# Optimization experiments

Hardware: AMD Instinct MI355X
Metric: run time of the kernel (lower is better)

The kernel has to match this reference:

```python
import jax, jax.numpy as jnp
import numpy as np

B, N, D_MODEL, N_HEADS, WINDOW = 2, 2048, 1024, 16, 512
HEAD_DIM = D_MODEL // N_HEADS

def setup_inputs() -> dict:
    key = jax.random.key(0)
    k1, k2, k3 = jax.random.split(key, 3)
    x = jax.random.normal(k1, (B, N, D_MODEL), dtype=jnp.float32)
    W_qkv = jax.random.normal(k2, (D_MODEL, 3 * D_MODEL), dtype=jnp.float32) * 0.02
    W_proj = jax.random.normal(k3, (D_MODEL, D_MODEL), dtype=jnp.float32) * 0.02
    b_proj = jnp.zeros((D_MODEL,), dtype=jnp.float32)
    return {"x": x, "W_qkv": W_qkv, "W_proj": W_proj, "b_proj": b_proj}

def reference(x, W_qkv, W_proj, b_proj):
    Bx, Nx, C = x.shape
    H, Dh = N_HEADS, C // N_HEADS
    scale = Dh ** -0.5
    window = min(WINDOW, Nx)
    half = window // 2
    # qkv: [B,N,3C] -> [3,B,H,N,Dh]
    qkv = (x @ W_qkv).reshape(Bx, Nx, 3, H, Dh).transpose(2, 0, 3, 1, 4)
    q, k, v = qkv[0], qkv[1], qkv[2]
    # banded mask: allowed iff i-half <= j <= i+half
    i = jnp.arange(Nx)[:, None]
    j = jnp.arange(Nx)[None, :]
    allowed = jnp.abs(i - j) <= half  # [N,N] bool
    attn = jnp.einsum('bhqd,bhkd->bhqk', q, k) * scale
    attn = jnp.where(allowed[None, None], attn, -jnp.inf)
    attn = jax.nn.softmax(attn, axis=-1)
    out = jnp.einsum('bhqk,bhkd->bhqd', attn, v)
    out = out.transpose(0, 2, 1, 3).reshape(Bx, Nx, C)
    return out @ W_proj + b_proj
```

## Files before the change

### kernel.cpp

```cpp
#include <hip/hip_runtime.h>
#include <stdint.h>


typedef _Float16 f16x8 __attribute__((ext_vector_type(8)));
typedef _Float16 f16x4 __attribute__((ext_vector_type(4)));
typedef __fp16   fp16x2n __attribute__((ext_vector_type(2)));
typedef float    f32x2 __attribute__((ext_vector_type(2)));
typedef float    f32x4 __attribute__((ext_vector_type(4)));
typedef float    f32x16 __attribute__((ext_vector_type(16)));

#define MFMA16(a, b, c) __builtin_amdgcn_mfma_f32_16x16x32_f16((a), (b), (c), 0, 0, 0)
#define MFMA32(a, b, c) __builtin_amdgcn_mfma_f32_32x32x16_f16((a), (b), (c), 0, 0, 0)

__device__ __forceinline__ void gload16(const void* g, void* l) {
  __builtin_amdgcn_global_load_lds(
      (const __attribute__((address_space(1))) void*)g,
      (__attribute__((address_space(3))) void*)l, 16, 0, 0);
}

__device__ __forceinline__ unsigned pk2(float a, float b) {
  fp16x2n t = __builtin_amdgcn_cvt_pkrtz(a, b);
  return __builtin_bit_cast(unsigned, t);
}

__global__ __launch_bounds__(256) void prep(const float* __restrict__ x,
                                            const float* __restrict__ wqkv,
                                            const float* __restrict__ wproj,
                                            _Float16* __restrict__ Xb,
                                            _Float16* __restrict__ Wqt,
                                            _Float16* __restrict__ Wpt) {
  __shared__ float t[64][65];
  const int id = blockIdx.x, tid = threadIdx.x;
  if (id < 4096) {
    int i = (id * 256 + tid) * 4;
    float4 v = *(const float4*)(x + i);
    f16x4 h;
    h[0] = (_Float16)v.x; h[1] = (_Float16)v.y;
    h[2] = (_Float16)v.z; h[3] = (_Float16)v.w;
    *(f16x4*)(Xb + i) = h;
    return;
  }
  const float* in; _Float16* out; int N, bx, by;
  if (id < 4864) { int tt = id - 4096; in = wqkv; out = Wqt; N = 3072; bx = tt % 48; by = tt / 48; }
  else           { int tt = id - 4864; in = wproj; out = Wpt; N = 1024; bx = tt & 15; by = tt >> 4; }
  const int n0 = bx * 64, k0 = by * 64;
  {
    int j = tid & 63;
#pragma unroll
    for (int p = 0; p < 16; p++) {
      int i = p * 4 + (tid >> 6);
      t[i][j] = in[(size_t)(k0 + i) * N + n0 + j];
    }
  }
  __syncthreads();
  {
    int i = tid & 63;
#pragma unroll
    for (int p = 0; p < 16; p++) {
      int j = p * 4 + (tid >> 6);
      out[(size_t)(n0 + j) * 1024 + k0 + i] = (_Float16)t[i][j];
    }
  }
}

template <int BM, int BN, int EPI>
__global__ __launch_bounds__(256) void gemm16(const _Float16* __restrict__ A,
                                              const _Float16* __restrict__ Bt,
                                              const int K,
                                              _Float16* __restrict__ oh,
                                              _Float16* __restrict__ vt,
                                              float* __restrict__ of,
                                              const float* __restrict__ bias,
                                              const int Nout) {
  constexpr int RF = BM / 32, CF = BN / 32;
  constexpr int SLABS = (BM + BN) / 8;
  __shared__ __align__(16) char smem[(BM + BN) * 128];
  char* As = smem;
  char* Bs = smem + BM * 128;
  const int tid = threadIdx.x, wave = tid >> 6, lane = tid & 63;
  const int il = lane & 15, ih = lane >> 4;
  const int bm = blockIdx.y * BM, bn = blockIdx.x * BN;
  const int wm = wave >> 1, wn = wave & 1;
  const int rs = lane >> 3, cp = lane & 7;

  f32x4 acc[RF][CF] = {};

  for (int k0 = 0; k0 < K; k0 += 64) {
    __syncthreads();
#pragma unroll
    for (int s0 = 0; s0 < SLABS / 4; s0++) {
      int s = wave + s0 * 4;
      int row = s * 8 + rs;
      int c = cp ^ (row & 7);
      if (row < BM)
        gload16(A + (size_t)(bm + row) * K + k0 + c * 8, As + s * 1024);
      else
        gload16(Bt + (size_t)(bn + row - BM) * K + k0 + c * 8, smem + s * 1024);
    }
    __syncthreads();
#pragma unroll
    for (int ks = 0; ks < 2; ks++) {
      f16x8 af[RF], bf[CF];
#pragma unroll
      for (int rf = 0; rf < RF; rf++) {
        int R = wm * (BM / 2) + rf * 16 + il;
        af[rf] = *(const f16x8*)(As + R * 128 + (((ks * 4 + ih) ^ (R & 7)) * 16));
      }
#pragma unroll
      for (int cf = 0; cf < CF; cf++) {
        int C = wn * (BN / 2) + cf * 16 + il;
        bf[cf] = *(const f16x8*)(Bs + C * 128 + (((ks * 4 + ih) ^ (C & 7)) * 16));
      }
#pragma unroll
      for (int rf = 0; rf < RF; rf++)
#pragma unroll
        for (int cf = 0; cf < CF; cf++)
          acc[rf][cf] = MFMA16(af[rf], bf[cf], acc[rf][cf]);
    }
  }

#pragma unroll
  for (int rf = 0; rf < RF; rf++)
#pragma unroll
    for (int cf = 0; cf < CF; cf++) {
      int row0 = bm + wm * (BM / 2) + rf * 16 + ih * 4;
      int col = bn + wn * (BN / 2) + cf * 16 + il;
      if (EPI == 0) {
        int sec = col >> 10, cc = col & 1023;
        if (sec == 2) {
          int b = row0 >> 11, n = row0 & 2047;
          int bh = b * 16 + (cc >> 6), dh = cc & 63;
          union { f16x4 h; uint2 u; } pk;
#pragma unroll
          for (int r = 0; r < 4; r++) pk.h[r] = (_Float16)acc[rf][cf][r];
          *(uint2*)(vt + (size_t)bh * 131072 + (size_t)dh * 2048 + n) = pk.u;
        } else {
#pragma unroll
          for (int r = 0; r < 4; r++) {
            int row = row0 + r;
            float v = acc[rf][cf][r];
            if (sec == 0) v *= 0.18033688f;
            size_t plane = (size_t)(sec * 32 + (row >> 11) * 16 + (cc >> 6));
            oh[plane * 131072 + (size_t)(row & 2047) * 64 + (cc & 63)] = (_Float16)v;
          }
        }
      } else {
#pragma unroll
        for (int r = 0; r < 4; r++)
          of[(size_t)(row0 + r) * Nout + col] = acc[rf][cf][r] + bias[col];
      }
    }
}

__global__ __launch_bounds__(512) void attn(const _Float16* __restrict__ QKV,
                                            const _Float16* __restrict__ VT,
                                            _Float16* __restrict__ O2) {
  __shared__ __align__(16) char smem[51200];
  const int tid = threadIdx.x, wave = tid >> 6, lane = tid & 63;
  const int qw = wave >> 1, sh = wave & 1;
  const int cl = lane & 31, hl = lane >> 5;
  const int rs = lane >> 3, cp = lane & 7;
  const int q0 = blockIdx.x * 128, bh = blockIdx.y;
  const _Float16* Qg = QKV + (size_t)bh * 131072;
  const _Float16* Kg = QKV + 4194304 + (size_t)bh * 131072;
  const _Float16* Vg = VT + (size_t)bh * 131072;
  const int t0 = (q0 >= 256) ? q0 - 256 : 0;
  const int t1 = (q0 + 384 <= 2048) ? q0 + 384 : 2048;
  const int niter = (t1 - t0) >> 6;

#pragma unroll
  for (int q = 0; q < 2; q++) {
    int s = 2 * wave + q;
    int row = s * 8 + rs;
    int c = cp ^ (row & 7);
    gload16(Qg + (size_t)(q0 + row) * 64 + c * 8, smem + s * 1024);
  }
  {
    char* B0 = smem + 18432;
    int row = wave * 8 + rs;
    int c = cp ^ (row & 7);
    gload16(Kg + (size_t)(t0 + row) * 64 + c * 8, B0 + wave * 1024);
    gload16(Vg + (size_t)row * 2048 + t0 + c * 8, B0 + 8192 + wave * 1024);
  }
  __syncthreads();

  f16x8 bq[4];
  {
    int row = 32 * qw + cl;
#pragma unroll
    for (int ks = 0; ks < 4; ks++)
      bq[ks] = *(const f16x8*)(smem + row * 128 + (((ks * 2 + hl) ^ (row & 7)) * 16));
  }

  f32x16 oacc[2] = {};
  float l_acc = 0.f;
  const int a0 = q0 + 32 * qw;

  for (int i = 0; i < niter; i++) {
    const int kt = t0 + i * 64;
    char* Bc = smem + 18432 + (i & 1) * 16384;
    if (i + 1 < niter) {
      char* Bn = smem + 18432 + ((i + 1) & 1) * 16384;
      int row = wave * 8 + rs;
      int c = cp ^ (row & 7);
      gload16(Kg + (size_t)(kt + 64 + row) * 64 + c * 8, Bn + wave * 1024);
      gload16(Vg + (size_t)row * 2048 + (kt + 64) + c * 8, Bn + 8192 + wave * 1024);
    }
    const int d0 = a0 - (kt + 32 * sh);
    if (d0 < 288 && d0 > -288) {
      char* Ksm = Bc;
      char* Vsm = Bc + 8192;
      f32x16 st = {};
      {
        const int krow = 32 * sh + cl;
        __builtin_amdgcn_s_setprio(1);
#pragma unroll
        for (int ks = 0; ks < 4; ks++) {
          f16x8 ak = *(const f16x8*)(Ksm + krow * 128 + (((ks * 2 + hl) ^ (krow & 7)) * 16));
          st = MFMA32(ak, bq[ks], st);
        }
        __builtin_amdgcn_s_setprio(0);
      }
      unsigned w0a[4], w1a[4];
#pragma unroll
      for (int g = 0; g < 4; g++) {
        float v[4];
#pragma unroll
        for (int i2 = 0; i2 < 4; i2++) {
          float e = __builtin_amdgcn_exp2f(st[4 * g + i2]);
          int kl = 8 * g + 4 * hl + i2;
          if (d0 == 256) e = (cl <= kl) ? e : 0.f;
          else if (d0 == -256) e = (cl >= kl) ? e : 0.f;
          l_acc += e;
          v[i2] = e;
        }
        w0a[g] = pk2(v[0], v[1]);
        w1a[g] = pk2(v[2], v[3]);
      }
#pragma unroll
      for (int ks2 = 0; ks2 < 2; ks2++) {
        unsigned kA0 = w0a[2 * ks2],     kA1 = w1a[2 * ks2];
        unsigned kB0 = w0a[2 * ks2 + 1], kB1 = w1a[2 * ks2 + 1];
        unsigned keep0 = hl ? kB0 : kA0, keep1 = hl ? kB1 : kA1;
        unsigned send0 = hl ? kA0 : kB0, send1 = hl ? kA1 : kB1;
        unsigned r0 = (unsigned)__shfl_xor((int)send0, 32);
        unsigned r1 = (unsigned)__shfl_xor((int)send1, 32);
        union { unsigned u[4]; f16x8 h; } bp;
        bp.u[0] = hl ? r0 : keep0;
        bp.u[1] = hl ? r1 : keep1;
        bp.u[2] = hl ? keep0 : r0;
        bp.u[3] = hl ? keep1 : r1;
        __builtin_amdgcn_s_setprio(1);
#pragma unroll
        for (int db = 0; db < 2; db++) {
          int vrow = 32 * db + cl;
          f16x8 av = *(const f16x8*)(Vsm + vrow * 128 +
                                     (((4 * sh + 2 * ks2 + hl) ^ (vrow & 7)) * 16));
          oacc[db] = MFMA32(av, bp.h, oacc[db]);
        }
        __builtin_amdgcn_s_setprio(0);
      }
    }
    __syncthreads();
  }

  const float lp = l_acc + __shfl_xor(l_acc, 32);
  char* Mq = smem + qw * 8448;
  if (sh == 1) {
#pragma unroll
    for (int db = 0; db < 2; db++)
#pragma unroll
      for (int g = 0; g < 4; g++) {
        int dh0 = 32 * db + 8 * g + 4 * hl;
        f32x2 a = {oacc[db][4 * g + 0], oacc[db][4 * g + 1]};
        f32x2 b = {oacc[db][4 * g + 2], oacc[db][4 * g + 3]};
        *(f32x2*)(Mq + cl * 264 + dh0 * 4) = a;
        *(f32x2*)(Mq + cl * 264 + dh0 * 4 + 8) = b;
      }
    if (hl == 0) *(float*)(smem + 34816 + (qw * 32 + cl) * 4) = lp;
  }
  __syncthreads();
  if (sh == 0) {
    float lo = *(const float*)(smem + 34816 + (qw * 32 + cl) * 4);
    float inv = 1.0f / (lp + lo);
    const int b = bh >> 4, h = bh & 15;
    _Float16* dst = O2 + (size_t)(b * 2048 + a0 + cl) * 1024 + h * 64;
#pragma unroll
    for (int db = 0; db < 2; db++)
#pragma unroll
      for (int g = 0; g < 4; g++) {
        int dh0 = 32 * db + 8 * g + 4 * hl;
        f32x2 a = *(const f32x2*)(Mq + cl * 264 + dh0 * 4);
        f32x2 b2 = *(const f32x2*)(Mq + cl * 264 + dh0 * 4 + 8);
        uint2 pkd = {pk2((oacc[db][4 * g + 0] + a[0]) * inv,
                         (oacc[db][4 * g + 1] + a[1]) * inv),
                     pk2((oacc[db][4 * g + 2] + b2[0]) * inv,
                         (oacc[db][4 * g + 3] + b2[1]) * inv)};
        *(uint2*)(dst + dh0) = pkd;
      }
  }
}


extern "C" void kernel_launch(void* const* d_in, const int* in_sizes, int n_in,
                              void* d_out, int out_size, void* d_ws, size_t ws_size,
                              hipStream_t stream) {
  const float* x = (const float*)d_in[0];
  const float* wqkv = (const float*)d_in[1];
  const float* wproj = (const float*)d_in[2];
  const float* bproj = (const float*)d_in[3];
  float* out = (float*)d_out;
  char* ws = (char*)d_ws;

  _Float16* Xb  = (_Float16*)(ws);
  _Float16* Wqt = (_Float16*)(ws + (size_t)(8  << 20));
  _Float16* Wpt = (_Float16*)(ws + (size_t)(14 << 20));
  _Float16* QKV = (_Float16*)(ws + (size_t)(16 << 20));
  _Float16* Vt  = (_Float16*)(ws + (size_t)(40 << 20));
  _Float16* O2  = (_Float16*)(ws);

  prep<<<5120, 256, 0, stream>>>(x, wqkv, wproj, Xb, Wqt, Wpt);
  gemm16<128, 128, 0><<<dim3(24, 32), 256, 0, stream>>>(Xb, Wqt, 1024, QKV, Vt,
                                                        nullptr, nullptr, 0);
  attn<<<dim3(16, 32), 512, 0, stream>>>(QKV, Vt, O2);
  gemm16<128, 64, 1><<<dim3(16, 32), 256, 0, stream>>>(O2, Wpt, 1024, nullptr,
                                                       nullptr, out, bproj, 1024);
}
```

Baseline: 155.5 us.

## Deepen K/V prefetch to two tiles ahead with a four-slot LDS ring

```diff
diff --git a/kernel.cpp b/kernel.cpp
--- a/kernel.cpp
+++ b/kernel.cpp
@@ -155,7 +155,7 @@
 __global__ __launch_bounds__(512) void attn(const _Float16* __restrict__ QKV,
                                             const _Float16* __restrict__ VT,
                                             _Float16* __restrict__ O2) {
-  __shared__ __align__(16) char smem[51200];
+  __shared__ __align__(16) char smem[65536];
   const int tid = threadIdx.x, wave = tid >> 6, lane = tid & 63;
   const int qw = wave >> 1, sh = wave & 1;
   const int cl = lane & 31, hl = lane >> 5;
@@ -167,6 +167,8 @@
   const int t0 = (q0 >= 256) ? q0 - 256 : 0;
   const int t1 = (q0 + 384 <= 2048) ? q0 + 384 : 2048;
   const int niter = (t1 - t0) >> 6;
+  const int srow = wave * 8 + rs;
+  const int sc = cp ^ (srow & 7);
 
 #pragma unroll
   for (int q = 0; q < 2; q++) {
@@ -176,11 +178,12 @@
     gload16(Qg + (size_t)(q0 + row) * 64 + c * 8, smem + s * 1024);
   }
   {
-    char* B0 = smem + 18432;
-    int row = wave * 8 + rs;
-    int c = cp ^ (row & 7);
-    gload16(Kg + (size_t)(t0 + row) * 64 + c * 8, B0 + wave * 1024);
-    gload16(Vg + (size_t)row * 2048 + t0 + c * 8, B0 + 8192 + wave * 1024);
+    char* B1 = smem + 16384;
+    gload16(Kg + (size_t)(t0 + srow) * 64 + sc * 8, B1 + wave * 1024);
+    gload16(Vg + (size_t)srow * 2048 + t0 + sc * 8, B1 + 8192 + wave * 1024);
+    char* B2 = smem + 32768;
+    gload16(Kg + (size_t)(t0 + 64 + srow) * 64 + sc * 8, B2 + wave * 1024);
+    gload16(Vg + (size_t)srow * 2048 + (t0 + 64) + sc * 8, B2 + 8192 + wave * 1024);
   }
   __syncthreads();
 
@@ -191,6 +194,7 @@
     for (int ks = 0; ks < 4; ks++)
       bq[ks] = *(const f16x8*)(smem + row * 128 + (((ks * 2 + hl) ^ (row & 7)) * 16));
   }
+  asm volatile("s_waitcnt lgkmcnt(0)" ::: "memory");
 
   f32x16 oacc[2] = {};
   float l_acc = 0.f;
@@ -198,16 +202,21 @@
 
   for (int i = 0; i < niter; i++) {
     const int kt = t0 + i * 64;
-    char* Bc = smem + 18432 + (i & 1) * 16384;
-    if (i + 1 < niter) {
-      char* Bn = smem + 18432 + ((i + 1) & 1) * 16384;
-      int row = wave * 8 + rs;
-      int c = cp ^ (row & 7);
-      gload16(Kg + (size_t)(kt + 64 + row) * 64 + c * 8, Bn + wave * 1024);
-      gload16(Vg + (size_t)row * 2048 + (kt + 64) + c * 8, Bn + 8192 + wave * 1024);
-    }
+    if (i + 2 < niter) {
+      char* Bn = smem + (((i + 3) & 3) * 16384);
+      gload16(Kg + (size_t)(kt + 128 + srow) * 64 + sc * 8, Bn + wave * 1024);
+      gload16(Vg + (size_t)srow * 2048 + (kt + 128) + sc * 8, Bn + 8192 + wave * 1024);
+      asm volatile("s_waitcnt vmcnt(4)" ::: "memory");
+    } else if (i + 1 < niter) {
+      asm volatile("s_waitcnt vmcnt(2)" ::: "memory");
+    } else {
+      asm volatile("s_waitcnt vmcnt(0)" ::: "memory");
+    }
+    __builtin_amdgcn_s_barrier();
+    __builtin_amdgcn_sched_barrier(0);
     const int d0 = a0 - (kt + 32 * sh);
     if (d0 < 288 && d0 > -288) {
+      char* Bc = smem + (((i + 1) & 3) * 16384);
       char* Ksm = Bc;
       char* Vsm = Bc + 8192;
       f32x16 st = {};
@@ -261,8 +270,9 @@
         __builtin_amdgcn_s_setprio(0);
       }
     }
-    __syncthreads();
-  }
+    __builtin_amdgcn_sched_barrier(0);
+  }
+  __syncthreads();
 
   const float lp = l_acc + __shfl_xor(l_acc, 32);
   char* Mq = smem + qw * 8448;
```

New measurement: 162.9 us. 4.8% more time.

## Replace QKV GEMM with 256x256-tile 8-wave ping-pong pipelined kernel

Applied to the files above, without the earlier changes.

```diff
diff --git a/kernel.cpp b/kernel.cpp
--- a/kernel.cpp
+++ b/kernel.cpp
@@ -61,6 +61,121 @@
       out[(size_t)(n0 + j) * 1024 + k0 + i] = (_Float16)t[i][j];
     }
   }
+}
+
+
+#define G8_READ_AF(AF, MG)                                                    \
+  _Pragma("unroll") for (int m = 0; m < 4; m++) {                             \
+    int R = wm * 128 + (MG) * 64 + m * 16 + il;                               \
+    _Pragma("unroll") for (int ks = 0; ks < 2; ks++)                          \
+        AF[m][ks] = *(const f16x8*)(Abuf + R * 128 +                          \
+                                    (((ks * 4 + ih) ^ (R & 7)) * 16));        \
+  }
+
+#define G8_READ_BF(BF, NG)                                                    \
+  _Pragma("unroll") for (int n = 0; n < 2; n++) {                             \
+    int C = wn * 64 + (NG) * 32 + n * 16 + il;                                \
+    _Pragma("unroll") for (int ks = 0; ks < 2; ks++)                          \
+        BF[n][ks] = *(const f16x8*)(Bbuf + C * 128 +                          \
+                                    (((ks * 4 + ih) ^ (C & 7)) * 16));        \
+  }
+
+#define G8_MFMA(AF, BF, MG, NG)                                               \
+  __builtin_amdgcn_s_barrier();                                               \
+  asm volatile("s_waitcnt lgkmcnt(0)" ::: "memory");                          \
+  __builtin_amdgcn_sched_barrier(0);                                          \
+  __builtin_amdgcn_s_setprio(1);                                              \
+  _Pragma("unroll") for (int m = 0; m < 4; m++)                               \
+      _Pragma("unroll") for (int n = 0; n < 2; n++)                           \
+          _Pragma("unroll") for (int ks = 0; ks < 2; ks++)                    \
+              acc[(MG) * 4 + m][(NG) * 2 + n] = MFMA16(                       \
+                  AF[m][ks], BF[n][ks], acc[(MG) * 4 + m][(NG) * 2 + n]);     \
+  __builtin_amdgcn_s_setprio(0);
+
+#define G8_STAGE_A(BUF, T)                                                    \
+  _Pragma("unroll") for (int hh = 0; hh < 4; hh++) {                          \
+    int row = hh * 64 + wave * 8 + rs;                                        \
+    int c = cp ^ (row & 7);                                                   \
+    gload16(A + (size_t)(bm + row) * 1024 + (T) * 64 + c * 8,                 \
+            smem + (BUF) * 65536 + hh * 8192 + wave * 1024);                  \
+  }
+
+#define G8_STAGE_B(BUF, T)                                                    \
+  _Pragma("unroll") for (int hh = 0; hh < 4; hh++) {                          \
+    int row = hh * 64 + wave * 8 + rs;                                        \
+    int c = cp ^ (row & 7);                                                   \
+    gload16(Bt + (size_t)(bn + row) * 1024 + (T) * 64 + c * 8,                \
+            smem + (BUF) * 65536 + 32768 + hh * 8192 + wave * 1024);          \
+  }
+
+__global__ __launch_bounds__(512, 2) void gemm8p(const _Float16* __restrict__ A,
+                                                 const _Float16* __restrict__ Bt,
+                                                 _Float16* __restrict__ oh,
+                                                 _Float16* __restrict__ vt) {
+  __shared__ __align__(16) char smem[131072];
+  const int tid = threadIdx.x, wave = tid >> 6, lane = tid & 63;
+  const int il = lane & 15, ih = lane >> 4;
+  const int rs = lane >> 3, cp = lane & 7;
+  const int bm = blockIdx.y * 256, bn = blockIdx.x * 256;
+  const int wm = wave >> 2, wn = wave & 3;
+
+  f32x4 acc[8][4] = {};
+
+  G8_STAGE_A(0, 0);
+  G8_STAGE_B(0, 0);
+  asm volatile("s_waitcnt vmcnt(0)" ::: "memory");
+  __syncthreads();
+
+  f16x8 af0[4][2], af1[4][2], bf0[2][2], bf1[2][2];
+#pragma unroll 1
+  for (int t = 0; t < 16; t++) {
+    const int cur = t & 1, nxt = cur ^ 1;
+    const char* Abuf = (const char*)smem + cur * 65536;
+    const char* Bbuf = Abuf + 32768;
+    const bool pf = (t + 1) < 16;
+    G8_READ_AF(af0, 0);
+    G8_READ_BF(bf0, 0);
+    if (pf) { G8_STAGE_A(nxt, t + 1); }
+    G8_MFMA(af0, bf0, 0, 0);
+    __builtin_amdgcn_s_barrier();
+    G8_READ_AF(af1, 1);
+    if (pf) { G8_STAGE_B(nxt, t + 1); }
+    G8_MFMA(af1, bf0, 1, 0);
+    __builtin_amdgcn_s_barrier();
+    G8_READ_BF(bf1, 1);
+    G8_MFMA(af1, bf1, 1, 1);
+    __builtin_amdgcn_s_barrier();
+    G8_READ_AF(af0, 0);
+    G8_MFMA(af0, bf1, 0, 1);
+    asm volatile("s_waitcnt vmcnt(0)" ::: "memory");
+    __builtin_amdgcn_s_barrier();
+  }
+
+#pragma unroll
+  for (int mi = 0; mi < 8; mi++)
+#pragma unroll
+    for (int ni = 0; ni < 4; ni++) {
+      int row0 = bm + wm * 128 + mi * 16 + ih * 4;
+      int col = bn + wn * 64 + ni * 16 + il;
+      int sec = col >> 10, cc = col & 1023;
+      if (sec == 2) {
+        int b = row0 >> 11, n = row0 & 2047;
+        int bh2 = b * 16 + (cc >> 6), dh = cc & 63;
+        union { f16x4 h; uint2 u; } pk;
+#pragma unroll
+        for (int r = 0; r < 4; r++) pk.h[r] = (_Float16)acc[mi][ni][r];
+        *(uint2*)(vt + (size_t)bh2 * 131072 + (size_t)dh * 2048 + n) = pk.u;
+      } else {
+#pragma unroll
+        for (int r = 0; r < 4; r++) {
+          int row = row0 + r;
+          float v = acc[mi][ni][r];
+          if (sec == 0) v *= 0.18033688f;
+          size_t plane = (size_t)(sec * 32 + (row >> 11) * 16 + (cc >> 6));
+          oh[plane * 131072 + (size_t)(row & 2047) * 64 + (cc & 63)] = (_Float16)v;
+        }
+      }
+    }
 }
 
 template <int BM, int BN, int EPI>
@@ -320,8 +435,7 @@
   _Float16* O2  = (_Float16*)(ws);
 
   prep<<<5120, 256, 0, stream>>>(x, wqkv, wproj, Xb, Wqt, Wpt);
-  gemm16<128, 128, 0><<<dim3(24, 32), 256, 0, stream>>>(Xb, Wqt, 1024, QKV, Vt,
-                                                        nullptr, nullptr, 0);
+  gemm8p<<<dim3(12, 16), 512, 0, stream>>>(Xb, Wqt, QKV, Vt);
   attn<<<dim3(16, 32), 512, 0, stream>>>(QKV, Vt, O2);
   gemm16<128, 64, 1><<<dim3(16, 32), 256, 0, stream>>>(O2, Wpt, 1024, nullptr,
                                                        nullptr, out, bproj, 1024);
```

New measurement: 164.2 us. 1.06x slower.

## Replace QKV GEMM with 8-wave 256x192 tile kernel using triple-buffered async loads

Applied to the files above, without the earlier changes.

```diff
diff --git a/kernel.cpp b/kernel.cpp
--- a/kernel.cpp
+++ b/kernel.cpp
@@ -61,6 +61,130 @@
       out[(size_t)(n0 + j) * 1024 + k0 + i] = (_Float16)t[i][j];
     }
   }
+}
+
+__global__ __launch_bounds__(512) void gemm8p(const _Float16* __restrict__ A,
+                                              const _Float16* __restrict__ Bt,
+                                              _Float16* __restrict__ oh,
+                                              _Float16* __restrict__ vt) {
+  __shared__ __align__(16) char smem[147456];
+  const int tid = threadIdx.x, wave = tid >> 6, lane = tid & 63;
+  const int il = lane & 15, ih = lane >> 4;
+  const int rs = lane >> 3, cp = lane & 7;
+  const int bm = blockIdx.y * 256, bn = blockIdx.x * 192;
+  const int wm = wave >> 2, wn = wave & 3;
+  const int srow = wave * 8 + rs;
+
+#define R15_STAGE_A(ABUF, T)                                                  \
+  _Pragma("unroll") for (int hh = 0; hh < 4; hh++) {                          \
+    int row = hh * 64 + srow;                                                 \
+    int c = cp ^ (row & 7);                                                   \
+    gload16(A + (size_t)(bm + row) * 1024 + (T) * 64 + c * 8,                 \
+            smem + (ABUF) * 32768 + hh * 8192 + wave * 1024);                 \
+  }
+#define R15_STAGE_B(BBUF, T)                                                  \
+  _Pragma("unroll") for (int hh = 0; hh < 3; hh++) {                          \
+    int row = hh * 64 + srow;                                                 \
+    int c = cp ^ (row & 7);                                                   \
+    gload16(Bt + (size_t)(bn + row) * 1024 + (T) * 64 + c * 8,                \
+            smem + 98304 + (BBUF) * 24576 + hh * 8192 + wave * 1024);         \
+  }
+
+  f32x4 acc[8][3] = {};
+
+  R15_STAGE_A(0, 0);
+  R15_STAGE_B(0, 0);
+  R15_STAGE_A(1, 1);
+  R15_STAGE_B(1, 1);
+  asm volatile("s_waitcnt vmcnt(7)" ::: "memory");
+  __builtin_amdgcn_s_barrier();
+
+  int ta = 0, sa = 2;
+#pragma unroll 1
+  for (int t = 0; t < 16; t++) {
+    const char* Abuf = (const char*)smem + ta * 32768;
+    const char* Bbuf = (const char*)smem + 98304 + (t & 1) * 24576;
+    f16x8 af[4][2], ag[4][2], bf[3][2];
+#pragma unroll
+    for (int m = 0; m < 4; m++) {
+      int R = wm * 128 + m * 16 + il;
+#pragma unroll
+      for (int ks = 0; ks < 2; ks++)
+        af[m][ks] = *(const f16x8*)(Abuf + R * 128 + (((ks * 4 + ih) ^ (R & 7)) * 16));
+    }
+#pragma unroll
+    for (int n = 0; n < 3; n++) {
+      int C = wn * 48 + n * 16 + il;
+#pragma unroll
+      for (int ks = 0; ks < 2; ks++)
+        bf[n][ks] = *(const f16x8*)(Bbuf + C * 128 + (((ks * 4 + ih) ^ (C & 7)) * 16));
+    }
+    if (t < 14) { R15_STAGE_A(sa, t + 2); }
+    asm volatile("s_waitcnt lgkmcnt(0)" ::: "memory");
+    __builtin_amdgcn_s_barrier();
+    __builtin_amdgcn_s_setprio(1);
+#pragma unroll
+    for (int m = 0; m < 4; m++)
+#pragma unroll
+      for (int n = 0; n < 3; n++)
+#pragma unroll
+        for (int ks = 0; ks < 2; ks++)
+          acc[m][n] = MFMA16(af[m][ks], bf[n][ks], acc[m][n]);
+    __builtin_amdgcn_s_setprio(0);
+#pragma unroll
+    for (int m = 0; m < 4; m++) {
+      int R = wm * 128 + 64 + m * 16 + il;
+#pragma unroll
+      for (int ks = 0; ks < 2; ks++)
+        ag[m][ks] = *(const f16x8*)(Abuf + R * 128 + (((ks * 4 + ih) ^ (R & 7)) * 16));
+    }
+    if (t < 14) { R15_STAGE_B(t & 1, t + 2); }
+    __builtin_amdgcn_s_setprio(1);
+#pragma unroll
+    for (int m = 0; m < 4; m++)
+#pragma unroll
+      for (int n = 0; n < 3; n++)
+#pragma unroll
+        for (int ks = 0; ks < 2; ks++)
+          acc[4 + m][n] = MFMA16(ag[m][ks], bf[n][ks], acc[4 + m][n]);
+    __builtin_amdgcn_s_setprio(0);
+    if (t <= 13) {
+      asm volatile("s_waitcnt vmcnt(7)" ::: "memory");
+    } else if (t == 14) {
+      asm volatile("s_waitcnt vmcnt(0)" ::: "memory");
+    }
+    if (t < 15) __builtin_amdgcn_s_barrier();
+    ta = (ta == 2) ? 0 : ta + 1;
+    sa = (sa == 2) ? 0 : sa + 1;
+  }
+
+#pragma unroll
+  for (int mi = 0; mi < 8; mi++)
+#pragma unroll
+    for (int ni = 0; ni < 3; ni++) {
+      int row0 = bm + wm * 128 + mi * 16 + ih * 4;
+      int col = bn + wn * 48 + ni * 16 + il;
+      int sec = col >> 10, cc = col & 1023;
+      if (sec == 2) {
+        int b = row0 >> 11, n = row0 & 2047;
+        int bh2 = b * 16 + (cc >> 6), dh = cc & 63;
+        union { f16x4 h; uint2 u; } pk;
+#pragma unroll
+        for (int r = 0; r < 4; r++) pk.h[r] = (_Float16)acc[mi][ni][r];
+        *(uint2*)(vt + (size_t)bh2 * 131072 + (size_t)dh * 2048 + n) = pk.u;
+      } else {
+#pragma unroll
+        for (int r = 0; r < 4; r++) {
+          int row = row0 + r;
+          float v = acc[mi][ni][r];
+          if (sec == 0) v *= 0.18033688f;
+          size_t plane = (size_t)(sec * 32 + (row >> 11) * 16 + (cc >> 6));
+          oh[plane * 131072 + (size_t)(row & 2047) * 64 + (cc & 63)] = (_Float16)v;
+        }
+      }
+    }
+#undef R15_STAGE_A
+#undef R15_STAGE_B
 }
 
 template <int BM, int BN, int EPI>
@@ -320,8 +444,7 @@
   _Float16* O2  = (_Float16*)(ws);
 
   prep<<<5120, 256, 0, stream>>>(x, wqkv, wproj, Xb, Wqt, Wpt);
-  gemm16<128, 128, 0><<<dim3(24, 32), 256, 0, stream>>>(Xb, Wqt, 1024, QKV, Vt,
-                                                        nullptr, nullptr, 0);
+  gemm8p<<<dim3(16, 16), 512, 0, stream>>>(Xb, Wqt, QKV, Vt);
   attn<<<dim3(16, 32), 512, 0, stream>>>(QKV, Vt, O2);
   gemm16<128, 64, 1><<<dim3(16, 32), 256, 0, stream>>>(O2, Wpt, 1024, nullptr,
                                                        nullptr, out, bproj, 1024);
```

After: 153.2 us. No clear change (-1.5%).
